# Optimization experiments

Hardware: AMD Instinct MI355X
Metric: run time of the kernel (lower is better)

The kernel has to match this reference:

```python
import jax, jax.numpy as jnp
import numpy as np
import math

N, C3, T = 32, 192, 2048  # C3 = 3 * head_dim

def setup_inputs() -> dict:
    key = jax.random.key(0)
    qkv = jax.random.normal(key, (N, C3, T), dtype=jnp.float32)
    return {"qkv": qkv}

def reference(qkv):
    ch = qkv.shape[1] // 3
    q, k, v = jnp.split(qkv, 3, axis=1)              # each [N, C, T]
    scale = 1.0 / math.sqrt(math.sqrt(ch))           # applied to both q and k
    # [N, T, T] attention scores
    weight = jnp.einsum('bct,bcs->bts', q * scale, k * scale)
    weight = jax.nn.softmax(weight.astype(jnp.float32), axis=-1).astype(qkv.dtype)
    # [N, C, T] output
    return jnp.einsum('bts,bcs->bct', weight, v)
```

## Files before the change

kernel.cpp:

```cpp
#include <hip/hip_runtime.h>

#define T_DIM 2048
#define D_DIM 64
#define NB 32

#define QT_OFF 0
#define KB_OFF 4194304
#define VB_OFF 8388608

typedef _Float16 half8 __attribute__((ext_vector_type(8)));
typedef _Float16 half4 __attribute__((ext_vector_type(4)));
typedef float f32x16 __attribute__((ext_vector_type(16)));
typedef float f32x4 __attribute__((ext_vector_type(4)));

#define ZERO16 (f32x16){0.f,0.f,0.f,0.f,0.f,0.f,0.f,0.f,0.f,0.f,0.f,0.f,0.f,0.f,0.f,0.f}

__global__ __launch_bounds__(256) void prepass(const float* __restrict__ qkv,
                                               _Float16* __restrict__ ws) {
  const int ttile = blockIdx.x;
  const int b = blockIdx.y;
  const int type = blockIdx.z;
  const int t0 = ttile * 64;
  __shared__ float Ls[64][65];

  const int tid = threadIdx.x;
  const int cc = tid >> 4;
  const int tt = (tid & 15) << 2;
  const float QS = 0.125f * 1.4426950408889634f;
  const float* src = qkv + ((size_t)b * 192 + type * 64) * T_DIM;
#pragma unroll
  for (int p = 0; p < 4; ++p) {
    const int c = p * 16 + cc;
    float4 v = *(const float4*)&src[(size_t)c * T_DIM + t0 + tt];
    if (type == 0) { v.x *= QS; v.y *= QS; v.z *= QS; v.w *= QS; }
    Ls[c][tt] = v.x; Ls[c][tt + 1] = v.y; Ls[c][tt + 2] = v.z; Ls[c][tt + 3] = v.w;
  }
  __syncthreads();

  if (type == 0) {
    const int t = tid >> 2, cg = (tid & 3) * 16;
    half8 h0, h1;
#pragma unroll
    for (int j = 0; j < 8; ++j) h0[j] = (_Float16)Ls[cg + j][t];
#pragma unroll
    for (int j = 0; j < 8; ++j) h1[j] = (_Float16)Ls[cg + 8 + j][t];
    _Float16* dst = ws + QT_OFF + ((size_t)b * T_DIM + t0 + t) * 64 + cg;
    *(half8*)dst = h0;
    *(half8*)(dst + 8) = h1;
  } else if (type == 1) {
    const int f = tid >> 6, h = (tid >> 5) & 1, s31 = tid & 31;
#pragma unroll
    for (int sbl = 0; sbl < 2; ++sbl) {
      const int sb = (t0 >> 5) + sbl;
      half8 hv;
#pragma unroll
      for (int j = 0; j < 8; ++j) hv[j] = (_Float16)Ls[f * 16 + h * 8 + j][sbl * 32 + s31];
      _Float16* dst = ws + KB_OFF + ((size_t)b * 64 + sb) * 2048 + f * 512 + h * 256 + s31 * 8;
      *(half8*)dst = hv;
    }
  } else {
#pragma unroll
    for (int p = 0; p < 2; ++p) {
      const int g = p * 256 + tid;
      const int sgl = g >> 6, c = g & 63;
      half8 hv;
#pragma unroll
      for (int j = 0; j < 8; ++j) hv[j] = (_Float16)Ls[c][sgl * 8 + j];
      _Float16* dst = ws + VB_OFF + (((size_t)b * 256 + (t0 >> 3) + sgl) * 64 + c) * 8;
      *(half8*)dst = hv;
    }
  }
}

__global__ __launch_bounds__(256, 2) void qkv_main(const _Float16* __restrict__ ws,
                                                   float* __restrict__ out) {
  const int tid = threadIdx.x;
  const int wave = tid >> 6, lane = tid & 63;
  const int l31 = lane & 31, h = lane >> 5;
  const int b = blockIdx.x & 31;
  const int qg = blockIdx.x >> 5;
  const int t0 = qg * 128 + wave * 32;

  const _Float16* Qt = ws + QT_OFF;
  const _Float16* kbase = ws + KB_OFF + (size_t)b * 131072;
  const _Float16* vbase = ws + VB_OFF + (size_t)b * 131072;

  const _Float16* qp = Qt + ((size_t)b * T_DIM + t0 + l31) * 64 + h * 8;
  half8 bq[4];
#pragma unroll
  for (int f = 0; f < 4; ++f) bq[f] = *(const half8*)(qp + f * 16);

  f32x16 o0 = ZERO16, o1 = ZERO16;
  float lp = 0.f;

  const _Float16* kp = kbase + h * 256 + l31 * 8;
  const _Float16* vp = vbase + l31 * 8 + h * 4;

  half8 ak[4];
#pragma unroll
  for (int f = 0; f < 4; ++f) ak[f] = *(const half8*)(kp + f * 512);

  for (int sb = 0; sb < 64; ++sb) {
    const _Float16* kn = kp + (size_t)(sb + 1 < 64 ? sb + 1 : sb) * 2048;
    half8 an0 = *(const half8*)(kn);
    half8 an1 = *(const half8*)(kn + 512);
    half8 an2 = *(const half8*)(kn + 1024);
    half8 an3 = *(const half8*)(kn + 1536);

    f32x16 s = ZERO16;
    s = __builtin_amdgcn_mfma_f32_32x32x16_f16(ak[0], bq[0], s, 0, 0, 0);
    s = __builtin_amdgcn_mfma_f32_32x32x16_f16(ak[1], bq[1], s, 0, 0, 0);
    s = __builtin_amdgcn_mfma_f32_32x32x16_f16(ak[2], bq[2], s, 0, 0, 0);
    s = __builtin_amdgcn_mfma_f32_32x32x16_f16(ak[3], bq[3], s, 0, 0, 0);

    const _Float16* vpi = vp + (size_t)sb * 2048;
    half4 bv[8];
#pragma unroll
    for (int g = 0; g < 4; ++g) {
      bv[2 * g] = *(const half4*)(vpi + g * 512);
      bv[2 * g + 1] = *(const half4*)(vpi + g * 512 + 256);
    }

    half4 ap[4];
#pragma unroll
    for (int g = 0; g < 4; ++g) {
      const float e0 = __builtin_amdgcn_exp2f(s[4 * g + 0]);
      const float e1 = __builtin_amdgcn_exp2f(s[4 * g + 1]);
      const float e2 = __builtin_amdgcn_exp2f(s[4 * g + 2]);
      const float e3 = __builtin_amdgcn_exp2f(s[4 * g + 3]);
      lp += (e0 + e1) + (e2 + e3);
      ap[g] = (half4){(_Float16)e0, (_Float16)e1, (_Float16)e2, (_Float16)e3};
    }

#pragma unroll
    for (int g = 0; g < 4; ++g) {
      o0 = __builtin_amdgcn_mfma_f32_32x32x8f16(ap[g], bv[2 * g], o0, 0, 0, 0);
      o1 = __builtin_amdgcn_mfma_f32_32x32x8f16(ap[g], bv[2 * g + 1], o1, 0, 0, 0);
    }

    ak[0] = an0; ak[1] = an1; ak[2] = an2; ak[3] = an3;
  }

  const float lf = lp + __shfl_xor(lp, 32);
  const float linv = 1.0f / lf;
  float* ob = out + (size_t)b * D_DIM * T_DIM;
#pragma unroll
  for (int g = 0; g < 4; ++g) {
    f32x4 r0, r1;
#pragma unroll
    for (int j = 0; j < 4; ++j) {
      const float il = __shfl(linv, g * 8 + h * 4 + j);
      r0[j] = o0[g * 4 + j] * il;
      r1[j] = o1[g * 4 + j] * il;
    }
    const int q = t0 + g * 8 + h * 4;
    *(f32x4*)&ob[(size_t)l31 * T_DIM + q] = r0;
    *(f32x4*)&ob[(size_t)(32 + l31) * T_DIM + q] = r1;
  }
}

extern "C" void kernel_launch(void* const* d_in, const int* in_sizes, int n_in,
                              void* d_out, int out_size, void* d_ws, size_t ws_size,
                              hipStream_t stream) {
  const float* qkv = (const float*)d_in[0];
  float* out = (float*)d_out;
  _Float16* ws = (_Float16*)d_ws;
  hipLaunchKernelGGL(prepass, dim3(32, 32, 3), dim3(256), 0, stream, qkv, ws);
  hipLaunchKernelGGL(qkv_main, dim3(512), dim3(256), 0, stream, ws, out);
}
```

Before: 140.9 us.

## Use 32x32x16 MFMA for PV via lane-shuffled P fragments and prefetch V

Replaces the eight 32x32x8 MFMAs of the P·V product with four 32x32x16 MFMAs. The probability fragments are regrouped across the two lane halves with xor-32 shuffles so each lane holds eight contiguous keys. V is now loaded as half8 and prefetched one iteration ahead, like K. The goal is fewer MFMA issues and hidden V load latency, at the cost of extra shuffles, selects and live registers.

```diff
diff --git a/kernel.cpp b/kernel.cpp
--- a/kernel.cpp
+++ b/kernel.cpp
@@ -72,6 +72,19 @@
   }
 }
 
+static __device__ __forceinline__ half4 shflx32(half4 x) {
+  int2 i = __builtin_bit_cast(int2, x);
+  i.x = __shfl_xor(i.x, 32);
+  i.y = __shfl_xor(i.y, 32);
+  return __builtin_bit_cast(half4, i);
+}
+static __device__ __forceinline__ half8 cat4(half4 lo, half4 hi) {
+  half8 r;
+  r[0] = lo[0]; r[1] = lo[1]; r[2] = lo[2]; r[3] = lo[3];
+  r[4] = hi[0]; r[5] = hi[1]; r[6] = hi[2]; r[7] = hi[3];
+  return r;
+}
+
 __global__ __launch_bounds__(256, 2) void qkv_main(const _Float16* __restrict__ ws,
                                                    float* __restrict__ out) {
   const int tid = threadIdx.x;
@@ -90,36 +103,39 @@
 #pragma unroll
   for (int f = 0; f < 4; ++f) bq[f] = *(const half8*)(qp + f * 16);
 
+  const f32x16 fz = ZERO16;
   f32x16 o0 = ZERO16, o1 = ZERO16;
   float lp = 0.f;
 
   const _Float16* kp = kbase + h * 256 + l31 * 8;
-  const _Float16* vp = vbase + l31 * 8 + h * 4;
+  const _Float16* vp = vbase + h * 512 + l31 * 8;
 
-  half8 ak[4];
+  half8 ak[4], bv[4];
 #pragma unroll
   for (int f = 0; f < 4; ++f) ak[f] = *(const half8*)(kp + f * 512);
+  bv[0] = *(const half8*)(vp);
+  bv[1] = *(const half8*)(vp + 256);
+  bv[2] = *(const half8*)(vp + 1024);
+  bv[3] = *(const half8*)(vp + 1280);
 
   for (int sb = 0; sb < 64; ++sb) {
-    const _Float16* kn = kp + (size_t)(sb + 1 < 64 ? sb + 1 : sb) * 2048;
+    const size_t nxt = (size_t)(sb + 1 < 64 ? sb + 1 : sb) * 2048;
+    const _Float16* kn = kp + nxt;
     half8 an0 = *(const half8*)(kn);
     half8 an1 = *(const half8*)(kn + 512);
     half8 an2 = *(const half8*)(kn + 1024);
     half8 an3 = *(const half8*)(kn + 1536);
+    const _Float16* vn = vp + nxt;
+    half8 bn0 = *(const half8*)(vn);
+    half8 bn1 = *(const half8*)(vn + 256);
+    half8 bn2 = *(const half8*)(vn + 1024);
+    half8 bn3 = *(const half8*)(vn + 1280);
 
-    f32x16 s = ZERO16;
-    s = __builtin_amdgcn_mfma_f32_32x32x16_f16(ak[0], bq[0], s, 0, 0, 0);
+    f32x16 s;
+    s = __builtin_amdgcn_mfma_f32_32x32x16_f16(ak[0], bq[0], fz, 0, 0, 0);
     s = __builtin_amdgcn_mfma_f32_32x32x16_f16(ak[1], bq[1], s, 0, 0, 0);
     s = __builtin_amdgcn_mfma_f32_32x32x16_f16(ak[2], bq[2], s, 0, 0, 0);
     s = __builtin_amdgcn_mfma_f32_32x32x16_f16(ak[3], bq[3], s, 0, 0, 0);
-
-    const _Float16* vpi = vp + (size_t)sb * 2048;
-    half4 bv[8];
-#pragma unroll
-    for (int g = 0; g < 4; ++g) {
-      bv[2 * g] = *(const half4*)(vpi + g * 512);
-      bv[2 * g + 1] = *(const half4*)(vpi + g * 512 + 256);
-    }
 
     half4 ap[4];
 #pragma unroll
@@ -132,13 +148,20 @@
       ap[g] = (half4){(_Float16)e0, (_Float16)e1, (_Float16)e2, (_Float16)e3};
     }
 
-#pragma unroll
-    for (int g = 0; g < 4; ++g) {
-      o0 = __builtin_amdgcn_mfma_f32_32x32x8f16(ap[g], bv[2 * g], o0, 0, 0, 0);
-      o1 = __builtin_amdgcn_mfma_f32_32x32x8f16(ap[g], bv[2 * g + 1], o1, 0, 0, 0);
-    }
+    const half4 xs0 = h ? ap[0] : ap[1];
+    const half4 ot0 = shflx32(xs0);
+    const half8 A0 = cat4(h ? ot0 : ap[0], h ? ap[1] : ot0);
+    const half4 xs1 = h ? ap[2] : ap[3];
+    const half4 ot1 = shflx32(xs1);
+    const half8 A1 = cat4(h ? ot1 : ap[2], h ? ap[3] : ot1);
+
+    o0 = __builtin_amdgcn_mfma_f32_32x32x16_f16(A0, bv[0], o0, 0, 0, 0);
+    o1 = __builtin_amdgcn_mfma_f32_32x32x16_f16(A0, bv[1], o1, 0, 0, 0);
+    o0 = __builtin_amdgcn_mfma_f32_32x32x16_f16(A1, bv[2], o0, 0, 0, 0);
+    o1 = __builtin_amdgcn_mfma_f32_32x32x16_f16(A1, bv[3], o1, 0, 0, 0);
 
     ak[0] = an0; ak[1] = an1; ak[2] = an2; ak[3] = an3;
+    bv[0] = bn0; bv[1] = bn1; bv[2] = bn2; bv[3] = bn3;
   }
 
   const float lf = lp + __shfl_xor(lp, 32);
```

After: 137.9 us. -2.2%, faster.
